# Performance work log

Measured on AMD Instinct MI355X. Metric: run time of the kernel, lower is better.

Reference implementation:

```python
import jax, jax.numpy as jnp
import numpy as np

BN_EPS = 1e-5

def _conv1d(x, w, b, pad):
    # x: [B, C_in, L], w: [C_out, C_in, K]
    y = jax.lax.conv_general_dilated(x, w, (1,), [(pad, pad)],
                                     dimension_numbers=('NCH', 'OIH', 'NCH'))
    return y + b[None, :, None]

def _gru_dir(x, wih, whh, bih, bhh, reverse):
    # x: [B, L, I]; wih: [3H, I]; whh: [3H, H] (PyTorch GRU gate order r,z,n)
    H = whh.shape[1]
    gx = jnp.einsum('bli,gi->blg', x, wih) + bih  # [B, L, 3H]
    gx = jnp.swapaxes(gx, 0, 1)                    # [L, B, 3H]
    if reverse:
        gx = gx[::-1]
    def step(h, xt):
        gh = h @ whh.T + bhh
        xr, xz, xn = jnp.split(xt, 3, axis=-1)
        hr, hz, hn = jnp.split(gh, 3, axis=-1)
        r = jax.nn.sigmoid(xr + hr)
        z = jax.nn.sigmoid(xz + hz)
        n = jnp.tanh(xn + r * hn)
        h = (1 - z) * n + z * h
        return h, h
    h0 = jnp.zeros((x.shape[0], H), x.dtype)
    _, hs = jax.lax.scan(step, h0, gx)
    if reverse:
        hs = hs[::-1]
    return jnp.swapaxes(hs, 0, 1)  # [B, L, H]

def _bigru(x, wih, whh, bih, bhh):
    f = _gru_dir(x, wih[0], whh[0], bih[0], bhh[0], False)
    b = _gru_dir(x, wih[1], whh[1], bih[1], bhh[1], True)
    return jnp.concatenate([f, b], axis=-1)

def _bn_eval(x, gamma, beta):
    # eval-mode BatchNorm1d with running_mean=0, running_var=1
    return x / jnp.sqrt(1.0 + BN_EPS) * gamma + beta

def _forward(wd_emb, pos_emb, conv_w2, conv_b2, conv_w3, conv_b3, conv_w4, conv_b4,
             wd_wih0, wd_whh0, wd_bih0, wd_bhh0, wd_wih1, wd_whh1, wd_bih1, wd_bhh1,
             pos_wih0, pos_whh0, pos_bih0, pos_bhh0, pos_wih1, pos_whh1, pos_bih1, pos_bhh1,
             squish_w, atten_proj, posfc_gamma, posfc_beta, posfc_w, posfc_b,
             fc1_w, fc1_b, fc_gamma, fc_beta, fc2_w, fc2_b, wd, pos):
    we = wd_emb[wd]    # [B, L, D]
    pe = pos_emb[pos]  # [B, L, D]
    x = jnp.swapaxes(we, 1, 2)  # [B, D, L]
    L = x.shape[-1]
    # parallel conv branches, truncated to min length L, concat -> 144 channels
    c2 = _conv1d(x, conv_w2, conv_b2, 1)[:, :, :L]
    c3 = _conv1d(x, conv_w3, conv_b3, 1)[:, :, :L]
    c4 = _conv1d(x, conv_w4, conv_b4, 2)[:, :, :L]
    feat = jnp.swapaxes(jnp.concatenate([c2, c3, c4], axis=1), 1, 2)  # [B, L, 144]
    # 2-layer bidirectional GRUs (hidden=3; dropout disabled at eval)
    wd_out = _bigru(_bigru(feat, wd_wih0, wd_whh0, wd_bih0, wd_bhh0),
                    wd_wih1, wd_whh1, wd_bih1, wd_bhh1)   # [B, L, 6]
    pos_out = _bigru(_bigru(pe, pos_wih0, pos_whh0, pos_bih0, pos_bhh0),
                     pos_wih1, pos_whh1, pos_bih1, pos_bhh1)  # [B, L, 6]
    # word attention (vectorized version of batch_matmul/attention_matmul loops)
    squish = jnp.tanh(wd_out @ squish_w)        # [B, L, 6]
    att = squish @ atten_proj                    # [B, L, 1]
    attn = jax.nn.softmax(att, axis=1)           # softmax over seq dim
    wd_atten = jnp.sum(wd_out * attn, axis=1)    # [B, 6]
    # auxiliary pos head
    ph = jax.nn.relu(_bn_eval(pos_out[:, -1, :], posfc_gamma, posfc_beta))
    auxi = jax.nn.softmax(ph @ posfc_w.T + posfc_b, axis=-1)  # [B, 3]
    # main head
    comb = jnp.concatenate([wd_atten, auxi], axis=1)  # [B, 9]
    h = jax.nn.relu(_bn_eval(comb @ fc1_w.T + fc1_b, fc_gamma, fc_beta))
    logits = jax.nn.softmax(h @ fc2_w.T + fc2_b, axis=-1)     # [B, 6]
    return logits, auxi

def setup_inputs() -> dict:
    key = jax.random.key(0)
    B, L, D, H, V, P = 512, 512, 100, 3, 23757, 57
    G = 3 * H  # 9
    keys = iter(jax.random.split(key, 48))
    def nrm(shape, s=0.1):
        return jax.random.normal(next(keys), shape, jnp.float32) * s
    inp = {}
    inp['wd'] = jax.random.randint(next(keys), (B, L), 0, V)
    inp['pos'] = jax.random.randint(next(keys), (B, L), 0, P)
    inp['wd_emb'] = nrm((V, D), 1.0)
    inp['pos_emb'] = nrm((P, D), 1.0)
    inp['conv_w2'] = nrm((48, D, 2)); inp['conv_b2'] = nrm((48,))
    inp['conv_w3'] = nrm((48, D, 3)); inp['conv_b3'] = nrm((48,))
    inp['conv_w4'] = nrm((48, D, 4)); inp['conv_b4'] = nrm((48,))
    inp['wd_wih0'] = nrm((2, G, 144)); inp['wd_whh0'] = nrm((2, G, H))
    inp['wd_bih0'] = nrm((2, G));      inp['wd_bhh0'] = nrm((2, G))
    inp['wd_wih1'] = nrm((2, G, 2 * H)); inp['wd_whh1'] = nrm((2, G, H))
    inp['wd_bih1'] = nrm((2, G));        inp['wd_bhh1'] = nrm((2, G))
    inp['pos_wih0'] = nrm((2, G, D));    inp['pos_whh0'] = nrm((2, G, H))
    inp['pos_bih0'] = nrm((2, G));       inp['pos_bhh0'] = nrm((2, G))
    inp['pos_wih1'] = nrm((2, G, 2 * H)); inp['pos_whh1'] = nrm((2, G, H))
    inp['pos_bih1'] = nrm((2, G));        inp['pos_bhh1'] = nrm((2, G))
    inp['squish_w'] = nrm((2 * H, 2 * H), 1.0)
    inp['atten_proj'] = nrm((2 * H, 1), 1.0)
    inp['posfc_gamma'] = jnp.ones((2 * H,), jnp.float32)
    inp['posfc_beta'] = jnp.zeros((2 * H,), jnp.float32)
    inp['posfc_w'] = nrm((3, 2 * H)); inp['posfc_b'] = nrm((3,))
    inp['fc1_w'] = nrm((128, 9)); inp['fc1_b'] = nrm((128,))
    inp['fc_gamma'] = jnp.ones((128,), jnp.float32)
    inp['fc_beta'] = jnp.zeros((128,), jnp.float32)
    inp['fc2_w'] = nrm((6, 128)); inp['fc2_b'] = nrm((6,))
    return inp

def reference(wd, pos, wd_emb, pos_emb, conv_w2, conv_b2, conv_w3, conv_b3, conv_w4, conv_b4,
              wd_wih0, wd_whh0, wd_bih0, wd_bhh0, wd_wih1, wd_whh1, wd_bih1, wd_bhh1,
              pos_wih0, pos_whh0, pos_bih0, pos_bhh0, pos_wih1, pos_whh1, pos_bih1, pos_bhh1,
              squish_w, atten_proj, posfc_gamma, posfc_beta, posfc_w, posfc_b,
              fc1_w, fc1_b, fc_gamma, fc_beta, fc2_w, fc2_b):
    return _forward(wd_emb, pos_emb, conv_w2, conv_b2, conv_w3, conv_b3, conv_w4, conv_b4,
                    wd_wih0, wd_whh0, wd_bih0, wd_bhh0, wd_wih1, wd_whh1, wd_bih1, wd_bhh1,
                    pos_wih0, pos_whh0, pos_bih0, pos_bhh0, pos_wih1, pos_whh1, pos_bih1, pos_bhh1,
                    squish_w, atten_proj, posfc_gamma, posfc_beta, posfc_w, posfc_b,
                    fc1_w, fc1_b, fc_gamma, fc_beta, fc2_w, fc2_b, wd, pos)
```

## Files before the change

kernel.cpp:

```cpp
#include <hip/hip_runtime.h>
#include <hip/hip_fp16.h>
#include <math.h>

#define BB 512
#define LL 512
#define VV 23757
#define PP 57

#define L2E  1.4426950408889634f
#define NL2E (-1.4426950408889634f)
#define TL2E 2.8853900817779268f

__device__ __forceinline__ float rcp_(float x) { return __builtin_amdgcn_rcpf(x); }
__device__ __forceinline__ float exp2_(float x) { return __builtin_amdgcn_exp2f(x); }
__device__ __forceinline__ float tanh_(float x) { return 1.f - 2.f * rcp_(exp2_(TL2E * x) + 1.f); }

__device__ __forceinline__ float gscale(int dg) {
    int g = (dg % 9) / 3;
    return g == 2 ? TL2E : NL2E;
}
__device__ __forceinline__ int is_rz(int dg) { return ((dg % 9) / 3) < 2; }

template <int K>
__device__ __forceinline__ float qb(float x) {
    constexpr int ctrl = K * 0x55;
    return __int_as_float(__builtin_amdgcn_update_dpp(0, __float_as_int(x), ctrl, 0xF, 0xF, true));
}

struct F3 { float r, z, n; };
struct H4 { __half2 a, b; };

__global__ void k_build_tables(const float* __restrict__ wd_wih0, const float* __restrict__ wd_bih0,
                               const float* __restrict__ wd_bhh0,
                               const float* __restrict__ cw2, const float* __restrict__ cb2,
                               const float* __restrict__ cw3, const float* __restrict__ cb3,
                               const float* __restrict__ cw4, const float* __restrict__ cb4,
                               const float* __restrict__ pos_emb,
                               const float* __restrict__ pos_wih0, const float* __restrict__ pos_bih0,
                               const float* __restrict__ pos_bhh0,
                               const float* __restrict__ wd_wih1, const float* __restrict__ wd_bih1,
                               const float* __restrict__ wd_bhh1,
                               const float* __restrict__ pos_wih1, const float* __restrict__ pos_bih1,
                               const float* __restrict__ pos_bhh1,
                               float* __restrict__ E, float* __restrict__ beff, float* __restrict__ Gp,
                               float* __restrict__ wih1t, float* __restrict__ bih1t)
{
    int idx = blockIdx.x * blockDim.x + threadIdx.x;
    if (idx < 7200) {
        int d  = idx % 100;
        int tt = (idx / 100) % 4;
        int dg = idx / 400;
        const float* wih = wd_wih0 + dg * 144;
        float acc = 0.f;
        if (tt == 0) {
            for (int o = 0; o < 48; ++o) acc += wih[96 + o] * cw4[o * 400 + d * 4 + 0];
        } else if (tt == 1) {
            for (int o = 0; o < 48; ++o) acc += wih[o]      * cw2[o * 200 + d * 2 + 0];
            for (int o = 0; o < 48; ++o) acc += wih[48 + o] * cw3[o * 300 + d * 3 + 0];
            for (int o = 0; o < 48; ++o) acc += wih[96 + o] * cw4[o * 400 + d * 4 + 1];
        } else if (tt == 2) {
            for (int o = 0; o < 48; ++o) acc += wih[o]      * cw2[o * 200 + d * 2 + 1];
            for (int o = 0; o < 48; ++o) acc += wih[48 + o] * cw3[o * 300 + d * 3 + 1];
            for (int o = 0; o < 48; ++o) acc += wih[96 + o] * cw4[o * 400 + d * 4 + 2];
        } else {
            for (int o = 0; o < 48; ++o) acc += wih[48 + o] * cw3[o * 300 + d * 3 + 2];
            for (int o = 0; o < 48; ++o) acc += wih[96 + o] * cw4[o * 400 + d * 4 + 3];
        }
        E[idx] = acc;
    } else if (idx < 7218) {
        int dg = idx - 7200;
        float acc = wd_bih0[dg];
        for (int o = 0; o < 48; ++o) acc += wd_wih0[dg * 144 + o]      * cb2[o];
        for (int o = 0; o < 48; ++o) acc += wd_wih0[dg * 144 + 48 + o] * cb3[o];
        for (int o = 0; o < 48; ++o) acc += wd_wih0[dg * 144 + 96 + o] * cb4[o];
        if (is_rz(dg)) acc += wd_bhh0[dg];
        beff[dg] = gscale(dg) * acc;
    } else if (idx < 8244) {
        int k = idx - 7218;
        int dg = k % 18;
        int p  = k / 18;
        float acc = pos_bih0[dg];
        for (int d = 0; d < 100; ++d) acc += pos_emb[p * 100 + d] * pos_wih0[dg * 100 + d];
        if (is_rz(dg)) acc += pos_bhh0[dg];
        Gp[p * 18 + dg] = gscale(dg) * acc;
    } else if (idx < 8352) {
        int i = idx - 8244; int dg = i / 6;
        wih1t[i] = gscale(dg) * wd_wih1[i];
    } else if (idx < 8370) {
        int dg = idx - 8352;
        float a = wd_bih1[dg] + (is_rz(dg) ? wd_bhh1[dg] : 0.f);
        bih1t[dg] = gscale(dg) * a;
    } else if (idx < 8478) {
        int i = idx - 8370; int dg = i / 6;
        wih1t[108 + i] = gscale(dg) * pos_wih1[i];
    } else if (idx < 8496) {
        int dg = idx - 8478;
        float a = pos_bih1[dg] + (is_rz(dg) ? pos_bhh1[dg] : 0.f);
        bih1t[18 + dg] = gscale(dg) * a;
    }
}

__global__ void __launch_bounds__(256) k_build_P(const float* __restrict__ wd_emb,
                                                 const float* __restrict__ E,
                                                 __half* __restrict__ P16)
{
    __shared__ float sEt[7200];
    for (int i = threadIdx.x; i < 7200; i += 256) {
        int d = i % 100, r = i / 100;
        int tt = r / 18, dg = r % 18;
        sEt[d * 72 + r] = E[dg * 400 + tt * 100 + d];
    }
    __syncthreads();
    int T = blockIdx.x * 256 + threadIdx.x;
    int og = T & 7;
    int vb = T >> 3;
    int v0 = vb * 4;
    if (v0 >= VV) return;
    int vlim = VV - 1 - v0;
    float gs[9];
#pragma unroll
    for (int k = 0; k < 9; ++k) {
        int dg = (og * 9 + k) % 18;
        gs[k] = ((dg % 9) / 3 == 2) ? TL2E : NL2E;
    }
    float acc[4][9];
#pragma unroll
    for (int vi = 0; vi < 4; ++vi)
#pragma unroll
        for (int k = 0; k < 9; ++k) acc[vi][k] = 0.f;

    const float* e0 = wd_emb + (size_t)v0 * 100;
#pragma unroll 1
    for (int d4 = 0; d4 < 25; ++d4) {
        float4 ev[4];
#pragma unroll
        for (int vi = 0; vi < 4; ++vi) {
            int vv = vi <= vlim ? vi : vlim;
            ev[vi] = *(const float4*)(e0 + vv * 100 + d4 * 4);
        }
#pragma unroll
        for (int dd = 0; dd < 4; ++dd) {
            int d = d4 * 4 + dd;
            const float* et = sEt + d * 72 + og * 9;
            float em0 = ((const float*)&ev[0])[dd];
            float em1 = ((const float*)&ev[1])[dd];
            float em2 = ((const float*)&ev[2])[dd];
            float em3 = ((const float*)&ev[3])[dd];
#pragma unroll
            for (int k = 0; k < 9; ++k) {
                float e = et[k];
                acc[0][k] = fmaf(em0, e, acc[0][k]);
                acc[1][k] = fmaf(em1, e, acc[1][k]);
                acc[2][k] = fmaf(em2, e, acc[2][k]);
                acc[3][k] = fmaf(em3, e, acc[3][k]);
            }
        }
    }
#pragma unroll
    for (int vi = 0; vi < 4; ++vi) {
        if (vi <= vlim) {
            __half* p = P16 + (size_t)(v0 + vi) * 72 + og * 9;
#pragma unroll
            for (int k = 0; k < 9; ++k) p[k] = __float2half_rn(gs[k] * acc[vi][k]);
        }
    }
}

__global__ void k_gather(const int* __restrict__ wd, const int* __restrict__ pos,
                         const __half* __restrict__ P16, const float* __restrict__ beff,
                         const float* __restrict__ Gp, char* __restrict__ gxh)
{
    int idx = blockIdx.x * blockDim.x + threadIdx.x;
    if (idx >= 2 * BB * LL) return;
    int branch = idx >= BB * LL;
    int k = idx - branch * BB * LL;
    int l = k % LL, b = k / LL;

    float v[18];
    if (!branch) {
#pragma unroll
        for (int i = 0; i < 18; ++i) v[i] = beff[i];
        const int* row = wd + b * LL;
#pragma unroll
        for (int t = 0; t < 4; ++t) {
            int ll = l - 2 + t;
            if (ll >= 0 && ll < LL) {
                const __half2* p = (const __half2*)(P16 + (size_t)row[ll] * 72 + t * 18);
#pragma unroll
                for (int i = 0; i < 9; ++i) {
                    float2 f = __half22float2(p[i]);
                    v[2 * i] += f.x;
                    v[2 * i + 1] += f.y;
                }
            }
        }
    } else {
        const float* p = Gp + pos[k] * 18;
#pragma unroll
        for (int i = 0; i < 18; ++i) v[i] = p[i];
    }
    char* g0 = gxh + ((size_t)((branch * 2 + 0) * BB + b) * LL + l) * 24;
    char* g1 = gxh + ((size_t)((branch * 2 + 1) * BB + b) * LL + l) * 24;
#pragma unroll
    for (int j = 0; j < 3; ++j) {
        H4 w0, w1;
        w0.a = __floats2half2_rn(v[j], v[3 + j]);
        w0.b = __floats2half2_rn(v[6 + j], 0.f);
        w1.a = __floats2half2_rn(v[9 + j], v[12 + j]);
        w1.b = __floats2half2_rn(v[15 + j], 0.f);
        *(H4*)(g0 + j * 8) = w0;
        *(H4*)(g1 + j * 8) = w1;
    }
}

#define GRU_CORE(GR, GZ, GN)                                                  \
    {                                                                         \
        float h0_ = qb<0>(h), h1_ = qb<1>(h), h2_ = qb<2>(h);                 \
        float sr_ = fmaf(wr0, h0_, fmaf(wr1, h1_, fmaf(wr2, h2_, (GR))));     \
        float sz_ = fmaf(wz0, h0_, fmaf(wz1, h1_, fmaf(wz2, h2_, (GZ))));     \
        float g3_ = fmaf(wn0, h0_, fmaf(wn1, h1_, fmaf(wn2, h2_, bnx)));      \
        float r_ = rcp_(1.f + exp2_(sr_));                                    \
        float z_ = rcp_(1.f + exp2_(sz_));                                    \
        float u_ = rcp_(1.f + exp2_(fmaf(r_, g3_, (GN))));                    \
        float n_ = fmaf(-2.f, u_, 1.f);                                       \
        h = fmaf(z_, h - n_, n_);                                             \
    }

__global__ void __launch_bounds__(64) k_scan0(
        const char* __restrict__ gxh, char* __restrict__ out0h,
        const float* __restrict__ whhA, const float* __restrict__ bhhA,
        const float* __restrict__ whhB, const float* __restrict__ bhhB)
{
    __shared__ float lbuf[8 * 81];
    int lane = threadIdx.x;
    int c = lane >> 2, sub = lane & 3;
    int jj = sub < 3 ? sub : 2;
    int chain = blockIdx.x;
    int branch = chain >> 10;
    int rem = chain & 1023;
    int dir = rem >> 9;

    const float* whh = (branch ? whhB : whhA) + dir * 27;
    const float* bhh = (branch ? bhhB : bhhA) + dir * 9;

    float wr0 = NL2E * whh[jj * 3 + 0], wr1 = NL2E * whh[jj * 3 + 1], wr2 = NL2E * whh[jj * 3 + 2];
    float wz0 = NL2E * whh[(3 + jj) * 3 + 0], wz1 = NL2E * whh[(3 + jj) * 3 + 1], wz2 = NL2E * whh[(3 + jj) * 3 + 2];
    float wn0 = TL2E * whh[(6 + jj) * 3 + 0], wn1 = TL2E * whh[(6 + jj) * 3 + 1], wn2 = TL2E * whh[(6 + jj) * 3 + 2];
    float bnx = TL2E * bhh[6 + jj];

    const int OMAX = 511 * 24;
    int t0 = c * 32 - 24;
    int sstp = dir ? -24 : 24;
    int off = dir ? (OMAX - t0 * 24) : t0 * 24;
    const char* gxc = gxh + (size_t)chain * (LL * 24) + jj * 8;

#define LDP(P) { int a_ = min(max(off, 0), OMAX); P = *(const H4*)(gxc + a_); off += sstp; }
    H4 p0, p1, p2, p3, p4, p5, p6, p7;
    LDP(p0) LDP(p1) LDP(p2) LDP(p3) LDP(p4) LDP(p5) LDP(p6) LDP(p7)

    char* ob = out0h + (size_t)chain * (LL * 8) + sub * 16;
    int wa = c * 5 + sub;

    float h = 0.f;
#define WSTEP(P) { H4 hv_ = P; LDP(P); float2 fa_ = __half22float2(hv_.a); \
                   float fn_ = __half22float2(hv_.b).x; GRU_CORE(fa_.x, fa_.y, fn_) }
#define RSTEP(P, S) { WSTEP(P) lbuf[(S) * 81 + wa] = h; }
#define FLUSH0(TB)                                                            \
    {                                                                         \
        int tbase = (TB);                                                     \
        int l0 = dir ? (LL - 1 - tbase - 7) : tbase;                          \
        _Pragma("unroll")                                                     \
        for (int i = 0; i < 2; ++i) {                                         \
            int lofs = sub * 2 + i;                                           \
            int s = dir ? (7 - lofs) : lofs;                                  \
            H4 hv;                                                            \
            hv.a = __floats2half2_rn(lbuf[s * 81 + c * 5 + 0],                \
                                     lbuf[s * 81 + c * 5 + 1]);               \
            hv.b = __floats2half2_rn(lbuf[s * 81 + c * 5 + 2],                \
                                     lbuf[s * 81 + c * 5 + 3]);               \
            *(H4*)(ob + (size_t)l0 * 8 + i * 8) = hv;                         \
        }                                                                     \
    }

    for (int g = 0; g < 3; ++g) {
        WSTEP(p0) WSTEP(p1) WSTEP(p2) WSTEP(p3) WSTEP(p4) WSTEP(p5) WSTEP(p6) WSTEP(p7)
    }
    h = c ? h : 0.f;

    for (int g = 0; g < 4; ++g) {
        RSTEP(p0, 0) RSTEP(p1, 1) RSTEP(p2, 2) RSTEP(p3, 3)
        RSTEP(p4, 4) RSTEP(p5, 5) RSTEP(p6, 6) RSTEP(p7, 7)
        FLUSH0(t0 + 24 + g * 8)
    }
#undef LDP
#undef WSTEP
#undef RSTEP
#undef FLUSH0
}

__global__ void __launch_bounds__(64) k_scan1(
        const char* __restrict__ out0h, char* __restrict__ out1h,
        const float* __restrict__ whhA, const float* __restrict__ bhhA,
        const float* __restrict__ whhB, const float* __restrict__ bhhB,
        const float* __restrict__ wih1t, const float* __restrict__ bih1t)
{
    __shared__ float lbuf[8 * 81];
    int lane = threadIdx.x;
    int c = lane >> 2, sub = lane & 3;
    int jj = sub < 3 ? sub : 2;
    int chain = blockIdx.x;
    int branch = chain >> 10;
    int rem = chain & 1023;
    int dir = rem >> 9;
    int b = rem & 511;

    const float* whh = (branch ? whhB : whhA) + dir * 27;
    const float* bhh = (branch ? bhhB : bhhA) + dir * 9;

    float wr0 = NL2E * whh[jj * 3 + 0], wr1 = NL2E * whh[jj * 3 + 1], wr2 = NL2E * whh[jj * 3 + 2];
    float wz0 = NL2E * whh[(3 + jj) * 3 + 0], wz1 = NL2E * whh[(3 + jj) * 3 + 1], wz2 = NL2E * whh[(3 + jj) * 3 + 2];
    float wn0 = TL2E * whh[(6 + jj) * 3 + 0], wn1 = TL2E * whh[(6 + jj) * 3 + 1], wn2 = TL2E * whh[(6 + jj) * 3 + 2];
    float bnx = TL2E * bhh[6 + jj];

    const float* Wb = wih1t + branch * 108;
    const float* Bv = bih1t + branch * 18;
    int dgr = dir * 9 + jj, dgz = dgr + 3, dgn = dgr + 6;
    float Wr0 = Wb[dgr * 6 + 0], Wr1 = Wb[dgr * 6 + 1], Wr2 = Wb[dgr * 6 + 2];
    float Wr3 = Wb[dgr * 6 + 3], Wr4 = Wb[dgr * 6 + 4], Wr5 = Wb[dgr * 6 + 5];
    float Wz0 = Wb[dgz * 6 + 0], Wz1 = Wb[dgz * 6 + 1], Wz2 = Wb[dgz * 6 + 2];
    float Wz3 = Wb[dgz * 6 + 3], Wz4 = Wb[dgz * 6 + 4], Wz5 = Wb[dgz * 6 + 5];
    float Wn0 = Wb[dgn * 6 + 0], Wn1 = Wb[dgn * 6 + 1], Wn2 = Wb[dgn * 6 + 2];
    float Wn3 = Wb[dgn * 6 + 3], Wn4 = Wb[dgn * 6 + 4], Wn5 = Wb[dgn * 6 + 5];
    float Br = Bv[dgr], Bz = Bv[dgz], Bn = Bv[dgn];

    const char* o0c = out0h + (size_t)((branch * 2 + 0) * BB + b) * (LL * 8);
    const char* o1c = out0h + (size_t)((branch * 2 + 1) * BB + b) * (LL * 8);

    const int OMAX = 511 * 8;
    int t0 = c * 32 - 24;
    int sstp = dir ? -8 : 8;
    int off = dir ? (OMAX - t0 * 8) : t0 * 8;

#define LDF(F, Q) { int a_ = min(max(off, 0), OMAX); F = *(const H4*)(o0c + a_); \
                    Q = *(const H4*)(o1c + a_); off += sstp; }
    H4 f0, f1, f2, f3, f4, f5, f6, f7;
    H4 q0, q1, q2, q3, q4, q5, q6, q7;
    LDF(f0, q0) LDF(f1, q1) LDF(f2, q2) LDF(f3, q3)
    LDF(f4, q4) LDF(f5, q5) LDF(f6, q6) LDF(f7, q7)

    char* ob = out1h + (size_t)chain * (LL * 8) + sub * 16;
    int wa = c * 5 + sub;

    float h = 0.f;
#define PRJ_STEP(FV, QV)                                                      \
    {                                                                         \
        float2 fa_ = __half22float2((FV).a);                                  \
        float fn_ = __half22float2((FV).b).x;                                 \
        float2 qa_ = __half22float2((QV).a);                                  \
        float qn_ = __half22float2((QV).b).x;                                 \
        float gr_ = fmaf(fa_.x, Wr0, fmaf(fa_.y, Wr1, fmaf(fn_, Wr2, Br)));   \
        gr_ = fmaf(qa_.x, Wr3, fmaf(qa_.y, Wr4, fmaf(qn_, Wr5, gr_)));        \
        float gz_ = fmaf(fa_.x, Wz0, fmaf(fa_.y, Wz1, fmaf(fn_, Wz2, Bz)));   \
        gz_ = fmaf(qa_.x, Wz3, fmaf(qa_.y, Wz4, fmaf(qn_, Wz5, gz_)));        \
        float gn_ = fmaf(fa_.x, Wn0, fmaf(fa_.y, Wn1, fmaf(fn_, Wn2, Bn)));   \
        gn_ = fmaf(qa_.x, Wn3, fmaf(qa_.y, Wn4, fmaf(qn_, Wn5, gn_)));        \
        GRU_CORE(gr_, gz_, gn_)                                               \
    }
#define WSTEP(F, Q) { H4 fv_ = F, qv_ = Q; LDF(F, Q); PRJ_STEP(fv_, qv_) }
#define RSTEP(F, Q, S) { WSTEP(F, Q) lbuf[(S) * 81 + wa] = h; }
#define FLUSH1(TB)                                                            \
    {                                                                         \
        int tbase = (TB);                                                     \
        int l0 = dir ? (LL - 1 - tbase - 7) : tbase;                          \
        _Pragma("unroll")                                                     \
        for (int i = 0; i < 2; ++i) {                                         \
            int lofs = sub * 2 + i;                                           \
            int s = dir ? (7 - lofs) : lofs;                                  \
            H4 hv;                                                            \
            hv.a = __floats2half2_rn(lbuf[s * 81 + c * 5 + 0],                \
                                     lbuf[s * 81 + c * 5 + 1]);               \
            hv.b = __floats2half2_rn(lbuf[s * 81 + c * 5 + 2],                \
                                     lbuf[s * 81 + c * 5 + 3]);               \
            *(H4*)(ob + (size_t)l0 * 8 + i * 8) = hv;                         \
        }                                                                     \
    }

    for (int g = 0; g < 3; ++g) {
        WSTEP(f0, q0) WSTEP(f1, q1) WSTEP(f2, q2) WSTEP(f3, q3)
        WSTEP(f4, q4) WSTEP(f5, q5) WSTEP(f6, q6) WSTEP(f7, q7)
    }
    h = c ? h : 0.f;

    for (int g = 0; g < 4; ++g) {
        RSTEP(f0, q0, 0) RSTEP(f1, q1, 1) RSTEP(f2, q2, 2) RSTEP(f3, q3, 3)
        RSTEP(f4, q4, 4) RSTEP(f5, q5, 5) RSTEP(f6, q6, 6) RSTEP(f7, q7, 7)
        FLUSH1(t0 + 24 + g * 8)
    }
#undef LDF
#undef PRJ_STEP
#undef WSTEP
#undef RSTEP
#undef FLUSH1
}

__global__ void k_head(const char* __restrict__ out1h,
                       const float* __restrict__ sw, const float* __restrict__ ap,
                       const float* __restrict__ pg, const float* __restrict__ pb,
                       const float* __restrict__ pw, const float* __restrict__ pbias,
                       const float* __restrict__ f1w, const float* __restrict__ f1b,
                       const float* __restrict__ fg, const float* __restrict__ fb,
                       const float* __restrict__ f2w, const float* __restrict__ f2b,
                       float* __restrict__ out)
{
    int b = blockIdx.x;
    int lane = threadIdx.x;
    __shared__ float ssw[36], sap[6], sph[6], scomb[9], sh[128], sl[6], se[6];
    const float BN = 0.9999950000374997f;

    if (lane < 36) ssw[lane] = sw[lane];
    if (lane < 6) {
        sap[lane] = ap[lane];
        H4 pf = *(const H4*)(out1h + ((size_t)((2 * BB) + b) * LL + 511) * 8);
        H4 pq = *(const H4*)(out1h + ((size_t)((3 * BB) + b) * LL + 511) * 8);
        float2 fa = __half22float2(pf.a); float fn = __half22float2(pf.b).x;
        float2 ba = __half22float2(pq.a); float bn = __half22float2(pq.b).x;
        float v = lane == 0 ? fa.x : lane == 1 ? fa.y : lane == 2 ? fn
                : lane == 3 ? ba.x : lane == 4 ? ba.y : bn;
        float x = v * BN * pg[lane] + pb[lane];
        sph[lane] = fmaxf(x, 0.f);
    }
    __syncthreads();

    const char* F = out1h + (size_t)b * (LL * 8);
    const char* Bw = out1h + (size_t)(BB + b) * (LL * 8);

    float att[8];
    float mx = -1e30f;
#pragma unroll
    for (int k = 0; k < 8; ++k) {
        int l = lane + 64 * k;
        H4 f4 = *(const H4*)(F + l * 8);
        H4 b4 = *(const H4*)(Bw + l * 8);
        float2 fa = __half22float2(f4.a); float fn = __half22float2(f4.b).x;
        float2 ba = __half22float2(b4.a); float bn = __half22float2(b4.b).x;
        float r0 = fa.x, r1 = fa.y, r2 = fn, r3 = ba.x, r4 = ba.y, r5 = bn;
        float a = 0.f;
#pragma unroll
        for (int j = 0; j < 6; ++j) {
            float s = r0 * ssw[0 * 6 + j] + r1 * ssw[1 * 6 + j] + r2 * ssw[2 * 6 + j] +
                      r3 * ssw[3 * 6 + j] + r4 * ssw[4 * 6 + j] + r5 * ssw[5 * 6 + j];
            a += sap[j] * tanh_(s);
        }
        att[k] = a;
        mx = fmaxf(mx, a);
    }
#pragma unroll
    for (int off = 32; off; off >>= 1) mx = fmaxf(mx, __shfl_xor(mx, off));
    float e[8];
    float sum = 0.f;
#pragma unroll
    for (int k = 0; k < 8; ++k) { e[k] = exp2_(L2E * (att[k] - mx)); sum += e[k]; }
#pragma unroll
    for (int off = 32; off; off >>= 1) sum += __shfl_xor(sum, off);

    float acc[6] = {0.f, 0.f, 0.f, 0.f, 0.f, 0.f};
#pragma unroll
    for (int k = 0; k < 8; ++k) {
        int l = lane + 64 * k;
        H4 f4 = *(const H4*)(F + l * 8);
        H4 b4 = *(const H4*)(Bw + l * 8);
        float2 fa = __half22float2(f4.a); float fn = __half22float2(f4.b).x;
        float2 ba = __half22float2(b4.a); float bn = __half22float2(b4.b).x;
        acc[0] += e[k] * fa.x; acc[1] += e[k] * fa.y; acc[2] += e[k] * fn;
        acc[3] += e[k] * ba.x; acc[4] += e[k] * ba.y; acc[5] += e[k] * bn;
    }
#pragma unroll
    for (int j = 0; j < 6; ++j) {
#pragma unroll
        for (int off = 32; off; off >>= 1) acc[j] += __shfl_xor(acc[j], off);
    }
    if (lane < 6) scomb[lane] = acc[lane] / sum;
    __syncthreads();

    if (lane == 0) {
        float a[3];
#pragma unroll
        for (int j = 0; j < 3; ++j) {
            float t = pbias[j];
#pragma unroll
            for (int i = 0; i < 6; ++i) t += sph[i] * pw[j * 6 + i];
            a[j] = t;
        }
        float m = fmaxf(a[0], fmaxf(a[1], a[2]));
        float e0 = exp2_(L2E * (a[0] - m)), e1 = exp2_(L2E * (a[1] - m)), e2 = exp2_(L2E * (a[2] - m));
        float s = e0 + e1 + e2;
        float x0 = e0 / s, x1 = e1 / s, x2 = e2 / s;
        scomb[6] = x0; scomb[7] = x1; scomb[8] = x2;
        out[BB * 6 + b * 3 + 0] = x0;
        out[BB * 6 + b * 3 + 1] = x1;
        out[BB * 6 + b * 3 + 2] = x2;
    }
    __syncthreads();
    for (int o = lane; o < 128; o += 64) {
        float t = f1b[o];
#pragma unroll
        for (int k = 0; k < 9; ++k) t += scomb[k] * f1w[o * 9 + k];
        float x = t * BN * fg[o] + fb[o];
        sh[o] = fmaxf(x, 0.f);
    }
    __syncthreads();
    if (lane < 6) {
        float t = f2b[lane];
        for (int k = 0; k < 128; ++k) t += sh[k] * f2w[lane * 128 + k];
        sl[lane] = t;
    }
    __syncthreads();
    if (lane < 6) {
        float m = sl[0];
#pragma unroll
        for (int j = 1; j < 6; ++j) m = fmaxf(m, sl[j]);
        se[lane] = exp2_(L2E * (sl[lane] - m));
    }
    __syncthreads();
    if (lane < 6) {
        float s = se[0] + se[1] + se[2] + se[3] + se[4] + se[5];
        out[b * 6 + lane] = se[lane] / s;
    }
}

extern "C" void kernel_launch(void* const* d_in, const int* in_sizes, int n_in,
                              void* d_out, int out_size, void* d_ws, size_t ws_size,
                              hipStream_t stream)
{
    const int* wd  = (const int*)d_in[0];
    const int* pos = (const int*)d_in[1];
    const float* wd_emb  = (const float*)d_in[2];
    const float* pos_emb = (const float*)d_in[3];
    const float* cw2 = (const float*)d_in[4];  const float* cb2 = (const float*)d_in[5];
    const float* cw3 = (const float*)d_in[6];  const float* cb3 = (const float*)d_in[7];
    const float* cw4 = (const float*)d_in[8];  const float* cb4 = (const float*)d_in[9];
    const float* wd_wih0 = (const float*)d_in[10]; const float* wd_whh0 = (const float*)d_in[11];
    const float* wd_bih0 = (const float*)d_in[12]; const float* wd_bhh0 = (const float*)d_in[13];
    const float* wd_wih1 = (const float*)d_in[14]; const float* wd_whh1 = (const float*)d_in[15];
    const float* wd_bih1 = (const float*)d_in[16]; const float* wd_bhh1 = (const float*)d_in[17];
    const float* pos_wih0 = (const float*)d_in[18]; const float* pos_whh0 = (const float*)d_in[19];
    const float* pos_bih0 = (const float*)d_in[20]; const float* pos_bhh0 = (const float*)d_in[21];
    const float* pos_wih1 = (const float*)d_in[22]; const float* pos_whh1 = (const float*)d_in[23];
    const float* pos_bih1 = (const float*)d_in[24]; const float* pos_bhh1 = (const float*)d_in[25];
    const float* squish_w   = (const float*)d_in[26];
    const float* atten_proj = (const float*)d_in[27];
    const float* posfc_gamma = (const float*)d_in[28]; const float* posfc_beta = (const float*)d_in[29];
    const float* posfc_w = (const float*)d_in[30]; const float* posfc_b = (const float*)d_in[31];
    const float* fc1_w = (const float*)d_in[32]; const float* fc1_b = (const float*)d_in[33];
    const float* fc_gamma = (const float*)d_in[34]; const float* fc_beta = (const float*)d_in[35];
    const float* fc2_w = (const float*)d_in[36]; const float* fc2_b = (const float*)d_in[37];

    float* ws = (float*)d_ws;
    size_t off = 0;
    __half* P16 = (__half*)(ws + off); off += (size_t)VV * 36 + 8;
    char* gxh = (char*)(ws + off);   off += (size_t)4 * BB * LL * 6;
    char* out0h = (char*)(ws + off); off += (size_t)4 * BB * LL * 2;
    char* out1h = (char*)(ws + off); off += (size_t)4 * BB * LL * 2;
    float* Etab = ws + off;   off += 7200;
    float* beff = ws + off;   off += 32;
    float* Gp = ws + off;     off += PP * 18 + 14;
    float* wih1t = ws + off;  off += 216;
    float* bih1t = ws + off;  off += 40;

    k_build_tables<<<(8496 + 255) / 256, 256, 0, stream>>>(
        wd_wih0, wd_bih0, wd_bhh0, cw2, cb2, cw3, cb3, cw4, cb4,
        pos_emb, pos_wih0, pos_bih0, pos_bhh0,
        wd_wih1, wd_bih1, wd_bhh1, pos_wih1, pos_bih1, pos_bhh1,
        Etab, beff, Gp, wih1t, bih1t);
    {
        int vb = (VV + 3) / 4;
        int threads = vb * 8;
        k_build_P<<<(threads + 255) / 256, 256, 0, stream>>>(wd_emb, Etab, P16);
    }
    k_gather<<<(2 * BB * LL + 255) / 256, 256, 0, stream>>>(wd, pos, P16, beff, Gp, gxh);
    k_scan0<<<2048, 64, 0, stream>>>(gxh, out0h, wd_whh0, wd_bhh0, pos_whh0, pos_bhh0);
    k_scan1<<<2048, 64, 0, stream>>>(out0h, out1h, wd_whh1, wd_bhh1, pos_whh1, pos_bhh1,
                                     wih1t, bih1t);
    k_head<<<BB, 64, 0, stream>>>(out1h, squish_w, atten_proj, posfc_gamma, posfc_beta,
                                  posfc_w, posfc_b, fc1_w, fc1_b, fc_gamma, fc_beta,
                                  fc2_w, fc2_b, (float*)d_out);
}
```

Measured before the change: 87.98 us.

## Fuse gather into layer-0 scan and stage scan inputs in LDS

Removes the separate gather kernel and its global gxh buffer. Each scan0 block now builds its chain's input-gate sequence directly into LDS, from the P16 table for the word branch or from a prepacked half-precision pos table. scan1 also stages the layer-0 outputs it needs into LDS, uses padded LDS addressing, and folds the layer-1 input weight scaling into the kernel instead of a prepass. This cuts a global write and read of the gate buffer and one kernel launch. In exchange, each scan block does redundant gather work per direction and has a larger LDS footprint, which may lower occupancy.

```diff
diff --git a/kernel.cpp b/kernel.cpp
--- a/kernel.cpp
+++ b/kernel.cpp
@@ -27,7 +27,6 @@
     return __int_as_float(__builtin_amdgcn_update_dpp(0, __float_as_int(x), ctrl, 0xF, 0xF, true));
 }
 
-struct F3 { float r, z, n; };
 struct H4 { __half2 a, b; };
 
 __global__ void k_build_tables(const float* __restrict__ wd_wih0, const float* __restrict__ wd_bih0,
@@ -38,12 +37,8 @@
                                const float* __restrict__ pos_emb,
                                const float* __restrict__ pos_wih0, const float* __restrict__ pos_bih0,
                                const float* __restrict__ pos_bhh0,
-                               const float* __restrict__ wd_wih1, const float* __restrict__ wd_bih1,
-                               const float* __restrict__ wd_bhh1,
-                               const float* __restrict__ pos_wih1, const float* __restrict__ pos_bih1,
-                               const float* __restrict__ pos_bhh1,
-                               float* __restrict__ E, float* __restrict__ beff, float* __restrict__ Gp,
-                               float* __restrict__ wih1t, float* __restrict__ bih1t)
+                               float* __restrict__ E, float* __restrict__ beff,
+                               char* __restrict__ Gp16)
 {
     int idx = blockIdx.x * blockDim.x + threadIdx.x;
     if (idx < 7200) {
@@ -75,28 +70,24 @@
         for (int o = 0; o < 48; ++o) acc += wd_wih0[dg * 144 + 96 + o] * cb4[o];
         if (is_rz(dg)) acc += wd_bhh0[dg];
         beff[dg] = gscale(dg) * acc;
-    } else if (idx < 8244) {
+    } else if (idx < 7560) {
         int k = idx - 7218;
-        int dg = k % 18;
-        int p  = k / 18;
-        float acc = pos_bih0[dg];
-        for (int d = 0; d < 100; ++d) acc += pos_emb[p * 100 + d] * pos_wih0[dg * 100 + d];
-        if (is_rz(dg)) acc += pos_bhh0[dg];
-        Gp[p * 18 + dg] = gscale(dg) * acc;
-    } else if (idx < 8352) {
-        int i = idx - 8244; int dg = i / 6;
-        wih1t[i] = gscale(dg) * wd_wih1[i];
-    } else if (idx < 8370) {
-        int dg = idx - 8352;
-        float a = wd_bih1[dg] + (is_rz(dg) ? wd_bhh1[dg] : 0.f);
-        bih1t[dg] = gscale(dg) * a;
-    } else if (idx < 8478) {
-        int i = idx - 8370; int dg = i / 6;
-        wih1t[108 + i] = gscale(dg) * pos_wih1[i];
-    } else if (idx < 8496) {
-        int dg = idx - 8478;
-        float a = pos_bih1[dg] + (is_rz(dg) ? pos_bhh1[dg] : 0.f);
-        bih1t[18 + dg] = gscale(dg) * a;
+        int j = k % 3;
+        int dirx = (k / 3) & 1;
+        int p = k / 6;
+        float g3[3];
+#pragma unroll
+        for (int g = 0; g < 3; ++g) {
+            int dg = dirx * 9 + g * 3 + j;
+            float acc = pos_bih0[dg];
+            for (int d = 0; d < 100; ++d) acc += pos_emb[p * 100 + d] * pos_wih0[dg * 100 + d];
+            if (g < 2) acc += pos_bhh0[dg];
+            g3[g] = (g == 2 ? TL2E : NL2E) * acc;
+        }
+        H4 w;
+        w.a = __floats2half2_rn(g3[0], g3[1]);
+        w.b = __floats2half2_rn(g3[2], 0.f);
+        *(H4*)(Gp16 + (size_t)(p * 6 + dirx * 3 + j) * 8) = w;
     }
 }
 
@@ -163,53 +154,6 @@
 #pragma unroll
             for (int k = 0; k < 9; ++k) p[k] = __float2half_rn(gs[k] * acc[vi][k]);
         }
-    }
-}
-
-__global__ void k_gather(const int* __restrict__ wd, const int* __restrict__ pos,
-                         const __half* __restrict__ P16, const float* __restrict__ beff,
-                         const float* __restrict__ Gp, char* __restrict__ gxh)
-{
-    int idx = blockIdx.x * blockDim.x + threadIdx.x;
-    if (idx >= 2 * BB * LL) return;
-    int branch = idx >= BB * LL;
-    int k = idx - branch * BB * LL;
-    int l = k % LL, b = k / LL;
-
-    float v[18];
-    if (!branch) {
-#pragma unroll
-        for (int i = 0; i < 18; ++i) v[i] = beff[i];
-        const int* row = wd + b * LL;
-#pragma unroll
-        for (int t = 0; t < 4; ++t) {
-            int ll = l - 2 + t;
-            if (ll >= 0 && ll < LL) {
-                const __half2* p = (const __half2*)(P16 + (size_t)row[ll] * 72 + t * 18);
-#pragma unroll
-                for (int i = 0; i < 9; ++i) {
-                    float2 f = __half22float2(p[i]);
-                    v[2 * i] += f.x;
-                    v[2 * i + 1] += f.y;
-                }
-            }
-        }
-    } else {
-        const float* p = Gp + pos[k] * 18;
-#pragma unroll
-        for (int i = 0; i < 18; ++i) v[i] = p[i];
-    }
-    char* g0 = gxh + ((size_t)((branch * 2 + 0) * BB + b) * LL + l) * 24;
-    char* g1 = gxh + ((size_t)((branch * 2 + 1) * BB + b) * LL + l) * 24;
-#pragma unroll
-    for (int j = 0; j < 3; ++j) {
-        H4 w0, w1;
-        w0.a = __floats2half2_rn(v[j], v[3 + j]);
-        w0.b = __floats2half2_rn(v[6 + j], 0.f);
-        w1.a = __floats2half2_rn(v[9 + j], v[12 + j]);
-        w1.b = __floats2half2_rn(v[15 + j], 0.f);
-        *(H4*)(g0 + j * 8) = w0;
-        *(H4*)(g1 + j * 8) = w1;
     }
 }
 
@@ -227,11 +171,14 @@
     }
 
 __global__ void __launch_bounds__(64) k_scan0(
-        const char* __restrict__ gxh, char* __restrict__ out0h,
+        const int* __restrict__ wd, const int* __restrict__ pos,
+        const __half* __restrict__ P16, const float* __restrict__ beff,
+        const char* __restrict__ Gp16, char* __restrict__ out0h,
         const float* __restrict__ whhA, const float* __restrict__ bhhA,
         const float* __restrict__ whhB, const float* __restrict__ bhhB)
 {
-    __shared__ float lbuf[8 * 81];
+    __shared__ char lgx[512 * 24 + 128];
+    __shared__ float lbuf[648];
     int lane = threadIdx.x;
     int c = lane >> 2, sub = lane & 3;
     int jj = sub < 3 ? sub : 2;
@@ -239,30 +186,74 @@
     int branch = chain >> 10;
     int rem = chain & 1023;
     int dir = rem >> 9;
+    int b = rem & 511;
+
+    if (branch == 0) {
+        const int* row = wd + b * LL;
+        float be[18];
+#pragma unroll
+        for (int i = 0; i < 18; ++i) be[i] = beff[i];
+        for (int r = lane; r < LL; r += 64) {
+            float v[18];
+#pragma unroll
+            for (int i = 0; i < 18; ++i) v[i] = be[i];
+#pragma unroll
+            for (int t = 0; t < 4; ++t) {
+                int ll = r - 2 + t;
+                if (ll >= 0 && ll < LL) {
+                    const __half2* p = (const __half2*)(P16 + (size_t)row[ll] * 72 + t * 18);
+#pragma unroll
+                    for (int i = 0; i < 9; ++i) {
+                        float2 f = __half22float2(p[i]);
+                        v[2 * i] += f.x; v[2 * i + 1] += f.y;
+                    }
+                }
+            }
+            int base = dir * 9;
+            int off = r * 24 + ((r >> 5) << 3);
+#pragma unroll
+            for (int j = 0; j < 3; ++j) {
+                H4 w;
+                w.a = __floats2half2_rn(v[base + j], v[base + 3 + j]);
+                w.b = __floats2half2_rn(v[base + 6 + j], 0.f);
+                *(H4*)(lgx + off + j * 8) = w;
+            }
+        }
+    } else {
+        const int* prow = pos + b * LL;
+        for (int r = lane; r < LL; r += 64) {
+            int p = prow[r];
+            const H4* src = (const H4*)(Gp16 + (size_t)(p * 6 + dir * 3) * 8);
+            int off = r * 24 + ((r >> 5) << 3);
+            H4 s0 = src[0], s1 = src[1], s2 = src[2];
+            *(H4*)(lgx + off + 0)  = s0;
+            *(H4*)(lgx + off + 8)  = s1;
+            *(H4*)(lgx + off + 16) = s2;
+        }
+    }
 
     const float* whh = (branch ? whhB : whhA) + dir * 27;
     const float* bhh = (branch ? bhhB : bhhA) + dir * 9;
-
     float wr0 = NL2E * whh[jj * 3 + 0], wr1 = NL2E * whh[jj * 3 + 1], wr2 = NL2E * whh[jj * 3 + 2];
     float wz0 = NL2E * whh[(3 + jj) * 3 + 0], wz1 = NL2E * whh[(3 + jj) * 3 + 1], wz2 = NL2E * whh[(3 + jj) * 3 + 2];
     float wn0 = TL2E * whh[(6 + jj) * 3 + 0], wn1 = TL2E * whh[(6 + jj) * 3 + 1], wn2 = TL2E * whh[(6 + jj) * 3 + 2];
     float bnx = TL2E * bhh[6 + jj];
 
-    const int OMAX = 511 * 24;
     int t0 = c * 32 - 24;
-    int sstp = dir ? -24 : 24;
-    int off = dir ? (OMAX - t0 * 24) : t0 * 24;
-    const char* gxc = gxh + (size_t)chain * (LL * 24) + jj * 8;
-
-#define LDP(P) { int a_ = min(max(off, 0), OMAX); P = *(const H4*)(gxc + a_); off += sstp; }
-    H4 p0, p1, p2, p3, p4, p5, p6, p7;
-    LDP(p0) LDP(p1) LDP(p2) LDP(p3) LDP(p4) LDP(p5) LDP(p6) LDP(p7)
+    int tv = t0;
+    int jj8 = jj * 8;
+
+#define LDP(P) { int tc = min(max(tv, 0), 511); int l = dir ? (511 - tc) : tc;    \
+                 int a_ = l * 24 + ((l >> 5) << 3) + jj8;                         \
+                 P = *(const H4*)(lgx + a_); ++tv; }
+    H4 p0, p1, p2, p3;
+    LDP(p0) LDP(p1) LDP(p2) LDP(p3)
 
     char* ob = out0h + (size_t)chain * (LL * 8) + sub * 16;
     int wa = c * 5 + sub;
 
     float h = 0.f;
-#define WSTEP(P) { H4 hv_ = P; LDP(P); float2 fa_ = __half22float2(hv_.a); \
+#define WSTEP(P) { H4 hv_ = P; LDP(P); float2 fa_ = __half22float2(hv_.a);        \
                    float fn_ = __half22float2(hv_.b).x; GRU_CORE(fa_.x, fa_.y, fn_) }
 #define RSTEP(P, S) { WSTEP(P) lbuf[(S) * 81 + wa] = h; }
 #define FLUSH0(TB)                                                            \
@@ -282,14 +273,12 @@
         }                                                                     \
     }
 
-    for (int g = 0; g < 3; ++g) {
-        WSTEP(p0) WSTEP(p1) WSTEP(p2) WSTEP(p3) WSTEP(p4) WSTEP(p5) WSTEP(p6) WSTEP(p7)
-    }
+    for (int g = 0; g < 6; ++g) { WSTEP(p0) WSTEP(p1) WSTEP(p2) WSTEP(p3) }
     h = c ? h : 0.f;
 
     for (int g = 0; g < 4; ++g) {
         RSTEP(p0, 0) RSTEP(p1, 1) RSTEP(p2, 2) RSTEP(p3, 3)
-        RSTEP(p4, 4) RSTEP(p5, 5) RSTEP(p6, 6) RSTEP(p7, 7)
+        RSTEP(p0, 4) RSTEP(p1, 5) RSTEP(p2, 6) RSTEP(p3, 7)
         FLUSH0(t0 + 24 + g * 8)
     }
 #undef LDP
@@ -302,9 +291,12 @@
         const char* __restrict__ out0h, char* __restrict__ out1h,
         const float* __restrict__ whhA, const float* __restrict__ bhhA,
         const float* __restrict__ whhB, const float* __restrict__ bhhB,
-        const float* __restrict__ wih1t, const float* __restrict__ bih1t)
+        const float* __restrict__ wihA, const float* __restrict__ bihA,
+        const float* __restrict__ wihB, const float* __restrict__ bihB)
 {
-    __shared__ float lbuf[8 * 81];
+    __shared__ char lf[512 * 8 + 128];
+    __shared__ char lq[512 * 8 + 128];
+    __shared__ float lbuf[648];
     int lane = threadIdx.x;
     int c = lane >> 2, sub = lane & 3;
     int jj = sub < 3 ? sub : 2;
@@ -314,39 +306,45 @@
     int dir = rem >> 9;
     int b = rem & 511;
 
+    {
+        const char* fg = out0h + (size_t)((branch * 2 + 0) * BB + b) * (LL * 8);
+        const char* qg = out0h + (size_t)((branch * 2 + 1) * BB + b) * (LL * 8);
+        for (int r = lane; r < LL; r += 64) {
+            int off = r * 8 + ((r >> 5) << 3);
+            *(H4*)(lf + off) = *(const H4*)(fg + r * 8);
+            *(H4*)(lq + off) = *(const H4*)(qg + r * 8);
+        }
+    }
+
     const float* whh = (branch ? whhB : whhA) + dir * 27;
     const float* bhh = (branch ? bhhB : bhhA) + dir * 9;
-
     float wr0 = NL2E * whh[jj * 3 + 0], wr1 = NL2E * whh[jj * 3 + 1], wr2 = NL2E * whh[jj * 3 + 2];
     float wz0 = NL2E * whh[(3 + jj) * 3 + 0], wz1 = NL2E * whh[(3 + jj) * 3 + 1], wz2 = NL2E * whh[(3 + jj) * 3 + 2];
     float wn0 = TL2E * whh[(6 + jj) * 3 + 0], wn1 = TL2E * whh[(6 + jj) * 3 + 1], wn2 = TL2E * whh[(6 + jj) * 3 + 2];
     float bnx = TL2E * bhh[6 + jj];
 
-    const float* Wb = wih1t + branch * 108;
-    const float* Bv = bih1t + branch * 18;
+    const float* wih = branch ? wihB : wihA;
+    const float* bih = branch ? bihB : bihA;
+    const float* bh1 = branch ? bhhB : bhhA;
     int dgr = dir * 9 + jj, dgz = dgr + 3, dgn = dgr + 6;
-    float Wr0 = Wb[dgr * 6 + 0], Wr1 = Wb[dgr * 6 + 1], Wr2 = Wb[dgr * 6 + 2];
-    float Wr3 = Wb[dgr * 6 + 3], Wr4 = Wb[dgr * 6 + 4], Wr5 = Wb[dgr * 6 + 5];
-    float Wz0 = Wb[dgz * 6 + 0], Wz1 = Wb[dgz * 6 + 1], Wz2 = Wb[dgz * 6 + 2];
-    float Wz3 = Wb[dgz * 6 + 3], Wz4 = Wb[dgz * 6 + 4], Wz5 = Wb[dgz * 6 + 5];
-    float Wn0 = Wb[dgn * 6 + 0], Wn1 = Wb[dgn * 6 + 1], Wn2 = Wb[dgn * 6 + 2];
-    float Wn3 = Wb[dgn * 6 + 3], Wn4 = Wb[dgn * 6 + 4], Wn5 = Wb[dgn * 6 + 5];
-    float Br = Bv[dgr], Bz = Bv[dgz], Bn = Bv[dgn];
-
-    const char* o0c = out0h + (size_t)((branch * 2 + 0) * BB + b) * (LL * 8);
-    const char* o1c = out0h + (size_t)((branch * 2 + 1) * BB + b) * (LL * 8);
-
-    const int OMAX = 511 * 8;
+    float Wr0 = NL2E * wih[dgr * 6 + 0], Wr1 = NL2E * wih[dgr * 6 + 1], Wr2 = NL2E * wih[dgr * 6 + 2];
+    float Wr3 = NL2E * wih[dgr * 6 + 3], Wr4 = NL2E * wih[dgr * 6 + 4], Wr5 = NL2E * wih[dgr * 6 + 5];
+    float Wz0 = NL2E * wih[dgz * 6 + 0], Wz1 = NL2E * wih[dgz * 6 + 1], Wz2 = NL2E * wih[dgz * 6 + 2];
+    float Wz3 = NL2E * wih[dgz * 6 + 3], Wz4 = NL2E * wih[dgz * 6 + 4], Wz5 = NL2E * wih[dgz * 6 + 5];
+    float Wn0 = TL2E * wih[dgn * 6 + 0], Wn1 = TL2E * wih[dgn * 6 + 1], Wn2 = TL2E * wih[dgn * 6 + 2];
+    float Wn3 = TL2E * wih[dgn * 6 + 3], Wn4 = TL2E * wih[dgn * 6 + 4], Wn5 = TL2E * wih[dgn * 6 + 5];
+    float Br = NL2E * (bih[dgr] + bh1[dgr]);
+    float Bz = NL2E * (bih[dgz] + bh1[dgz]);
+    float Bn = TL2E * bih[dgn];
+
     int t0 = c * 32 - 24;
-    int sstp = dir ? -8 : 8;
-    int off = dir ? (OMAX - t0 * 8) : t0 * 8;
-
-#define LDF(F, Q) { int a_ = min(max(off, 0), OMAX); F = *(const H4*)(o0c + a_); \
-                    Q = *(const H4*)(o1c + a_); off += sstp; }
-    H4 f0, f1, f2, f3, f4, f5, f6, f7;
-    H4 q0, q1, q2, q3, q4, q5, q6, q7;
+    int tv = t0;
+
+#define LDF(F, Q) { int tc = min(max(tv, 0), 511); int l = dir ? (511 - tc) : tc; \
+                    int a_ = l * 8 + ((l >> 5) << 3);                             \
+                    F = *(const H4*)(lf + a_); Q = *(const H4*)(lq + a_); ++tv; }
+    H4 f0, f1, f2, f3, q0, q1, q2, q3;
     LDF(f0, q0) LDF(f1, q1) LDF(f2, q2) LDF(f3, q3)
-    LDF(f4, q4) LDF(f5, q5) LDF(f6, q6) LDF(f7, q7)
 
     char* ob = out1h + (size_t)chain * (LL * 8) + sub * 16;
     int wa = c * 5 + sub;
@@ -385,15 +383,12 @@
         }                                                                     \
     }
 
-    for (int g = 0; g < 3; ++g) {
-        WSTEP(f0, q0) WSTEP(f1, q1) WSTEP(f2, q2) WSTEP(f3, q3)
-        WSTEP(f4, q4) WSTEP(f5, q5) WSTEP(f6, q6) WSTEP(f7, q7)
-    }
+    for (int g = 0; g < 6; ++g) { WSTEP(f0, q0) WSTEP(f1, q1) WSTEP(f2, q2) WSTEP(f3, q3) }
     h = c ? h : 0.f;
 
     for (int g = 0; g < 4; ++g) {
         RSTEP(f0, q0, 0) RSTEP(f1, q1, 1) RSTEP(f2, q2, 2) RSTEP(f3, q3, 3)
-        RSTEP(f4, q4, 4) RSTEP(f5, q5, 5) RSTEP(f6, q6, 6) RSTEP(f7, q7, 7)
+        RSTEP(f0, q0, 4) RSTEP(f1, q1, 5) RSTEP(f2, q2, 6) RSTEP(f3, q3, 7)
         FLUSH1(t0 + 24 + g * 8)
     }
 #undef LDF
@@ -558,29 +553,25 @@
     float* ws = (float*)d_ws;
     size_t off = 0;
     __half* P16 = (__half*)(ws + off); off += (size_t)VV * 36 + 8;
-    char* gxh = (char*)(ws + off);   off += (size_t)4 * BB * LL * 6;
     char* out0h = (char*)(ws + off); off += (size_t)4 * BB * LL * 2;
     char* out1h = (char*)(ws + off); off += (size_t)4 * BB * LL * 2;
     float* Etab = ws + off;   off += 7200;
     float* beff = ws + off;   off += 32;
-    float* Gp = ws + off;     off += PP * 18 + 14;
-    float* wih1t = ws + off;  off += 216;
-    float* bih1t = ws + off;  off += 40;
-
-    k_build_tables<<<(8496 + 255) / 256, 256, 0, stream>>>(
+    char* Gp16 = (char*)(ws + off); off += 704;
+
+    k_build_tables<<<(7560 + 255) / 256, 256, 0, stream>>>(
         wd_wih0, wd_bih0, wd_bhh0, cw2, cb2, cw3, cb3, cw4, cb4,
         pos_emb, pos_wih0, pos_bih0, pos_bhh0,
-        wd_wih1, wd_bih1, wd_bhh1, pos_wih1, pos_bih1, pos_bhh1,
-        Etab, beff, Gp, wih1t, bih1t);
+        Etab, beff, Gp16);
     {
         int vb = (VV + 3) / 4;
         int threads = vb * 8;
         k_build_P<<<(threads + 255) / 256, 256, 0, stream>>>(wd_emb, Etab, P16);
     }
-    k_gather<<<(2 * BB * LL + 255) / 256, 256, 0, stream>>>(wd, pos, P16, beff, Gp, gxh);
-    k_scan0<<<2048, 64, 0, stream>>>(gxh, out0h, wd_whh0, wd_bhh0, pos_whh0, pos_bhh0);
+    k_scan0<<<2048, 64, 0, stream>>>(wd, pos, P16, beff, Gp16, out0h,
+                                     wd_whh0, wd_bhh0, pos_whh0, pos_bhh0);
     k_scan1<<<2048, 64, 0, stream>>>(out0h, out1h, wd_whh1, wd_bhh1, pos_whh1, pos_bhh1,
-                                     wih1t, bih1t);
+                                     wd_wih1, wd_bih1, pos_wih1, pos_bih1);
     k_head<<<BB, 64, 0, stream>>>(out1h, squish_w, atten_proj, posfc_gamma, posfc_beta,
                                   posfc_w, posfc_b, fc1_w, fc1_b, fc_gamma, fc_beta,
                                   fc2_w, fc2_b, (float*)d_out);
```

New measurement: 97.04 us. +10.3%, slower.
